# Performance work log

Hardware: AMD Instinct MI355X
Metric: run time of the kernel (lower is better)

The kernel has to match this reference:

```python
import jax, jax.numpy as jnp
import numpy as np

DIM = 768
N_HEADS = 12
HEAD_DIM = DIM // N_HEADS
B, T = 2, 2048


def setup_inputs() -> dict:
    key = jax.random.key(0)
    ks = jax.random.split(key, 11)
    s = 0.02
    return {
        "q_in": jax.random.normal(ks[0], (B, T, DIM), jnp.float32),
        "k_in": jax.random.normal(ks[1], (B, T, DIM), jnp.float32),
        "v_in": jax.random.normal(ks[2], (B, T, DIM), jnp.float32),
        "Wq": jax.random.normal(ks[3], (DIM, DIM), jnp.float32) * s,
        "bq": jnp.zeros((DIM,), jnp.float32),
        "Wk": jax.random.normal(ks[4], (DIM, DIM), jnp.float32) * s,
        "bk": jnp.zeros((DIM,), jnp.float32),
        "Wv": jax.random.normal(ks[5], (DIM, DIM), jnp.float32) * s,
        "bv": jnp.zeros((DIM,), jnp.float32),
        "Wo": jax.random.normal(ks[6], (DIM, DIM), jnp.float32) * s,
        "bo": jnp.zeros((DIM,), jnp.float32),
    }


def reference(q_in, k_in, v_in, Wq, bq, Wk, bk, Wv, bv, Wo, bo):
    b, t, c = q_in.shape
    scale = HEAD_DIM ** -0.5
    # linear projections (torch Linear: x @ W.T + b)
    q = q_in @ Wq.T + bq
    k = k_in @ Wk.T + bk
    v = v_in @ Wv.T + bv
    # [b, t, h, d] -> [b, h, t, d]
    q = q.reshape(b, t, N_HEADS, HEAD_DIM).transpose(0, 2, 1, 3)
    k = k.reshape(b, t, N_HEADS, HEAD_DIM).transpose(0, 2, 1, 3)
    v = v.reshape(b, t, N_HEADS, HEAD_DIM).transpose(0, 2, 1, 3)
    scores = jnp.einsum("bhqd,bhkd->bhqk", q, k) * scale  # full TxT scores
    probs = jax.nn.softmax(scores, axis=-1)
    attn = jnp.einsum("bhqk,bhkd->bhqd", probs, v)
    attn = attn.transpose(0, 2, 1, 3).reshape(b, t, c)
    return attn @ Wo.T + bo
```

## Files before the change

kernel.cpp:

```cpp
#include <hip/hip_runtime.h>


typedef unsigned short u16;
typedef __attribute__((ext_vector_type(8))) short short8;
typedef __attribute__((ext_vector_type(4))) short short4v;
typedef __attribute__((ext_vector_type(4))) float float4v;

#define DIMC 768
#define NTOK 4096
#define NHD  12
#define HDD  64
#define SEQT 2048

#if __has_builtin(__builtin_amdgcn_mfma_f32_16x16x16bf16_1k)
#define HAVE_MFMA16 1
#else
#define HAVE_MFMA16 0
#endif

__device__ __forceinline__ u16 f2bf(float f) {
  union { float f; unsigned u; } v; v.f = f;
  unsigned r = v.u + 0x7fffu + ((v.u >> 16) & 1u);
  return (u16)(r >> 16);
}
__device__ __forceinline__ float bf2f(u16 u) {
  union { unsigned u; float f; } v; v.u = ((unsigned)u) << 16;
  return v.f;
}
__device__ __forceinline__ short4v u2s4(uint2 u) {
  union { uint2 u; short4v s; } v; v.u = u; return v.s;
}

__global__ __launch_bounds__(256) void cvt_all(
    const float* __restrict__ a0, const float* __restrict__ a1, const float* __restrict__ a2,
    const float* __restrict__ a3, const float* __restrict__ a4, const float* __restrict__ a5,
    const float* __restrict__ a6,
    u16* __restrict__ o0, u16* __restrict__ o1, u16* __restrict__ o2,
    u16* __restrict__ o3, u16* __restrict__ o4, u16* __restrict__ o5,
    u16* __restrict__ o6) {
  int bid = blockIdx.x;
  const float* s; u16* d; int inner;
  if (bid < 9216) {
    int z = bid / 3072; inner = bid - z * 3072;
    s = (z == 0) ? a0 : (z == 1) ? a1 : a2;
    d = (z == 0) ? o0 : (z == 1) ? o1 : o2;
  } else {
    int r = bid - 9216; int z = r / 576; inner = r - z * 576;
    s = (z == 0) ? a3 : (z == 1) ? a4 : (z == 2) ? a5 : a6;
    d = (z == 0) ? o3 : (z == 1) ? o4 : (z == 2) ? o5 : o6;
  }
  size_t i = ((size_t)inner * 256 + threadIdx.x) * 4;
  float4 v = *(const float4*)(s + i);
  *(ushort4*)(d + i) = make_ushort4(f2bf(v.x), f2bf(v.y), f2bf(v.z), f2bf(v.w));
}

__device__ __forceinline__ void gemm_mainloop3(
    const u16* __restrict__ X, const u16* __restrict__ W,
    int m0, int n0, u16* Als, u16* Bls, float4v acc[4][4]) {
  int tid = threadIdx.x;
  int sr = tid >> 3, sc = (tid & 7) * 8;
  int w = tid >> 6, lane = tid & 63, quad = lane >> 4, r15 = lane & 15;
  int wm = (w >> 1) * 64, wn = (w & 1) * 64;
  const u16* xp0 = X + (size_t)(m0 + sr) * DIMC + sc;
  const u16* xp1 = xp0 + 32 * DIMC;
  const u16* xp2 = xp0 + 64 * DIMC;
  const u16* xp3 = xp0 + 96 * DIMC;
  const u16* wp0 = W + (size_t)(n0 + sr) * DIMC + sc;
  const u16* wp1 = wp0 + 32 * DIMC;
  const u16* wp2 = wp0 + 64 * DIMC;
  const u16* wp3 = wp0 + 96 * DIMC;
  uint4 pa0 = *(const uint4*)xp0, pa1 = *(const uint4*)xp1;
  uint4 pa2 = *(const uint4*)xp2, pa3 = *(const uint4*)xp3;
  uint4 pb0 = *(const uint4*)wp0, pb1 = *(const uint4*)wp1;
  uint4 pb2 = *(const uint4*)wp2, pb3 = *(const uint4*)wp3;
  for (int k0 = 0; k0 < DIMC; k0 += 64) {
    __syncthreads();
    *(uint4*)(Als + sr * 72 + sc) = pa0;
    *(uint4*)(Als + (sr + 32) * 72 + sc) = pa1;
    *(uint4*)(Als + (sr + 64) * 72 + sc) = pa2;
    *(uint4*)(Als + (sr + 96) * 72 + sc) = pa3;
    *(uint4*)(Bls + sr * 72 + sc) = pb0;
    *(uint4*)(Bls + (sr + 32) * 72 + sc) = pb1;
    *(uint4*)(Bls + (sr + 64) * 72 + sc) = pb2;
    *(uint4*)(Bls + (sr + 96) * 72 + sc) = pb3;
    __syncthreads();
    int kn = k0 + 64;
    if (kn < DIMC) {
      pa0 = *(const uint4*)(xp0 + kn); pa1 = *(const uint4*)(xp1 + kn);
      pa2 = *(const uint4*)(xp2 + kn); pa3 = *(const uint4*)(xp3 + kn);
      pb0 = *(const uint4*)(wp0 + kn); pb1 = *(const uint4*)(wp1 + kn);
      pb2 = *(const uint4*)(wp2 + kn); pb3 = *(const uint4*)(wp3 + kn);
    }
    #pragma unroll
    for (int sk = 0; sk < 2; sk++) {
      short8 af[4], bf[4];
      #pragma unroll
      for (int mf = 0; mf < 4; mf++)
        af[mf] = *(const short8*)(Als + (wm + mf * 16 + r15) * 72 + sk * 32 + quad * 8);
      #pragma unroll
      for (int nf = 0; nf < 4; nf++)
        bf[nf] = *(const short8*)(Bls + (wn + nf * 16 + r15) * 72 + sk * 32 + quad * 8);
      #pragma unroll
      for (int mf = 0; mf < 4; mf++)
        #pragma unroll
        for (int nf = 0; nf < 4; nf++)
          acc[mf][nf] = __builtin_amdgcn_mfma_f32_16x16x32_bf16(af[mf], bf[nf], acc[mf][nf], 0, 0, 0);
    }
  }
}

__global__ __launch_bounds__(256, 2) void gemm_qkv(
    const u16* __restrict__ xq, const u16* __restrict__ xk, const u16* __restrict__ xv,
    const u16* __restrict__ wq, const u16* __restrict__ wk, const u16* __restrict__ wv,
    const float* __restrict__ bq, const float* __restrict__ bk, const float* __restrict__ bv,
    u16* __restrict__ Qh, u16* __restrict__ Kh, u16* __restrict__ Vt) {
  __shared__ __align__(16) u16 LS[2 * 128 * 72];
  u16* Als = LS;
  u16* Bls = LS + 128 * 72;
  int z = blockIdx.z;
  const u16* X = (z == 0) ? xq : (z == 1) ? xk : xv;
  const u16* W = (z == 0) ? wq : (z == 1) ? wk : wv;
  const float* bias = (z == 0) ? bq : (z == 1) ? bk : bv;
  int m0 = blockIdx.x * 128, n0 = blockIdx.y * 128;
  float4v acc[4][4];
  #pragma unroll
  for (int i = 0; i < 4; i++)
    #pragma unroll
    for (int j = 0; j < 4; j++)
      #pragma unroll
      for (int r = 0; r < 4; r++) acc[i][j][r] = 0.f;
  gemm_mainloop3(X, W, m0, n0, Als, Bls, acc);
  int tid = threadIdx.x, w = tid >> 6, lane = tid & 63, quad = lane >> 4, r15 = lane & 15;
  int wm = (w >> 1) * 64, wn = (w & 1) * 64;
  if (z == 2) {
    __syncthreads();
    u16* T = LS;
    #pragma unroll
    for (int mf = 0; mf < 4; mf++)
      #pragma unroll
      for (int nf = 0; nf < 4; nf++)
        #pragma unroll
        for (int rg = 0; rg < 4; rg++) {
          int mloc = wm + mf * 16 + quad * 4 + rg;
          int nloc = wn + nf * 16 + r15;
          T[nloc * 136 + mloc] = f2bf(acc[mf][nf][rg] + bias[n0 + nloc]);
        }
    __syncthreads();
    int r = tid >> 1, seg = tid & 1;
    int b = m0 >> 11, t0 = m0 & 2047;
    int h = (n0 + r) >> 6, d = (n0 + r) & 63;
    size_t base = (((size_t)(b * NHD + h)) * HDD + d) * SEQT + t0 + seg * 64;
    const u16* src = T + r * 136 + seg * 64;
    #pragma unroll
    for (int j = 0; j < 8; j++)
      *(uint4*)(Vt + base + j * 8) = *(const uint4*)(src + j * 8);
  } else {
    #pragma unroll
    for (int mf = 0; mf < 4; mf++)
      #pragma unroll
      for (int nf = 0; nf < 4; nf++)
        #pragma unroll
        for (int rg = 0; rg < 4; rg++) {
          int m = m0 + wm + mf * 16 + quad * 4 + rg;
          int n = n0 + wn + nf * 16 + r15;
          float val = acc[mf][nf][rg] + bias[n];
          if (z == 0) val *= 0.180336880f;
          int b = m >> 11, t = m & 2047, h = n >> 6, d = n & 63;
          u16 o = f2bf(val);
          size_t bh = (size_t)(b * NHD + h);
          if (z == 0) Qh[(bh * SEQT + t) * HDD + d] = o;
          else Kh[(bh * SEQT + t) * HDD + d] = o;
        }
  }
}

__global__ __launch_bounds__(256, 4) void attn_kernel(
    const u16* __restrict__ Qh, const u16* __restrict__ Kh, const u16* __restrict__ Vt,
    u16* __restrict__ Opart, float* __restrict__ Lpart) {
  __shared__ __align__(16) u16 Kls[64 * 64];
  __shared__ __align__(16) u16 Vls[64 * 64];
#if !HAVE_MFMA16
  __shared__ __align__(16) u16 Pls[4 * 32 * 64];
#endif
  int bh = blockIdx.y, sp = blockIdx.z, qt0 = blockIdx.x * 128;
  int tid = threadIdx.x, w = tid >> 6, lane = tid & 63, quad = lane >> 4, r15 = lane & 15;
  int qw = qt0 + w * 32;
  const int nt = 8;
  int kt0 = sp * (nt * 64);

  int rr = r15 & 7;
  int sx0 = (quad ^ rr) * 8;
  int sx1 = ((4 + quad) ^ rr) * 8;
  int q1 = quad >> 1, q0 = quad & 1;

  short8 qa[2][2];
  #pragma unroll
  for (int qs = 0; qs < 2; qs++) {
    const u16* qp = Qh + ((size_t)bh * SEQT + qw + qs * 16 + r15) * HDD + quad * 8;
    qa[qs][0] = *(const short8*)qp;
    qa[qs][1] = *(const short8*)(qp + 32);
  }
  float4v fzero;
  #pragma unroll
  for (int r = 0; r < 4; r++) fzero[r] = 0.f;

  float4v oacc[2][4];
  float lsum[2];
  #pragma unroll
  for (int qs = 0; qs < 2; qs++) {
    lsum[qs] = 0.f;
    #pragma unroll
    for (int dt = 0; dt < 4; dt++)
      #pragma unroll
      for (int r = 0; r < 4; r++) oacc[qs][dt][r] = 0.f;
  }

  const u16* Kbase = Kh + (size_t)bh * SEQT * HDD;
  const u16* Vbase = Vt + (size_t)bh * HDD * SEQT;
  int sr = tid >> 3, sc = (tid & 7) * 8;
  int sg = (((tid & 7) ^ (sr & 7)) * 8);

  uint4 pk0 = *(const uint4*)(Kbase + (size_t)(kt0 + sr) * HDD + sc);
  uint4 pk1 = *(const uint4*)(Kbase + (size_t)(kt0 + sr + 32) * HDD + sc);
  uint4 pv0 = *(const uint4*)(Vbase + (size_t)sr * SEQT + kt0 + sc);
  uint4 pv1 = *(const uint4*)(Vbase + (size_t)(sr + 32) * SEQT + kt0 + sc);

  for (int it = 0; it < nt; it++) {
    __syncthreads();
    *(uint4*)(Kls + sr * 64 + sg) = pk0;
    *(uint4*)(Kls + (sr + 32) * 64 + sg) = pk1;
    *(uint4*)(Vls + sr * 64 + sg) = pv0;
    *(uint4*)(Vls + (sr + 32) * 64 + sg) = pv1;
    __syncthreads();
    int nit = it + 1; if (nit == nt) nit = 0;
    int ktn = kt0 + nit * 64;
    pk0 = *(const uint4*)(Kbase + (size_t)(ktn + sr) * HDD + sc);
    pk1 = *(const uint4*)(Kbase + (size_t)(ktn + sr + 32) * HDD + sc);
    pv0 = *(const uint4*)(Vbase + (size_t)sr * SEQT + ktn + sc);
    pv1 = *(const uint4*)(Vbase + (size_t)(sr + 32) * SEQT + ktn + sc);

    __builtin_amdgcn_s_setprio(1);
#if HAVE_MFMA16
    #pragma unroll
    for (int nk = 0; nk < 4; nk++) {
      short8 k0 = *(const short8*)(Kls + (nk * 16 + r15) * 64 + sx0);
      short8 k1 = *(const short8*)(Kls + (nk * 16 + r15) * 64 + sx1);
      #pragma unroll
      for (int qs = 0; qs < 2; qs++) {
        float4v zv = __builtin_amdgcn_mfma_f32_16x16x32_bf16(k0, qa[qs][0], fzero, 0, 0, 0);
        zv = __builtin_amdgcn_mfma_f32_16x16x32_bf16(k1, qa[qs][1], zv, 0, 0, 0);
        float p0 = __builtin_amdgcn_exp2f(zv[0]);
        float p1 = __builtin_amdgcn_exp2f(zv[1]);
        float p2 = __builtin_amdgcn_exp2f(zv[2]);
        float p3 = __builtin_amdgcn_exp2f(zv[3]);
        lsum[qs] += (p0 + p1) + (p2 + p3);
        uint2 pw = make_uint2(
            __builtin_amdgcn_perm(__float_as_uint(p1), __float_as_uint(p0), 0x07060302u),
            __builtin_amdgcn_perm(__float_as_uint(p3), __float_as_uint(p2), 0x07060302u));
        short4v pb = u2s4(pw);
        #pragma unroll
        for (int dt = 0; dt < 4; dt++) {
          uint2 vw = *(const uint2*)(Vls + (dt * 16 + r15) * 64 +
                                     (((nk * 2 + q1) ^ rr) * 8) + q0 * 4);
          oacc[qs][dt] = __builtin_amdgcn_mfma_f32_16x16x16bf16_1k(
              u2s4(vw), pb, oacc[qs][dt], 0, 0, 0);
        }
      }
    }
#else
    u16* Pw = Pls + w * (32 * 64);
    #pragma unroll
    for (int nk = 0; nk < 4; nk++) {
      short8 k0 = *(const short8*)(Kls + (nk * 16 + r15) * 64 + sx0);
      short8 k1 = *(const short8*)(Kls + (nk * 16 + r15) * 64 + sx1);
      #pragma unroll
      for (int qs = 0; qs < 2; qs++) {
        float4v zv = __builtin_amdgcn_mfma_f32_16x16x32_bf16(k0, qa[qs][0], fzero, 0, 0, 0);
        zv = __builtin_amdgcn_mfma_f32_16x16x32_bf16(k1, qa[qs][1], zv, 0, 0, 0);
        float p0 = __builtin_amdgcn_exp2f(zv[0]);
        float p1 = __builtin_amdgcn_exp2f(zv[1]);
        float p2 = __builtin_amdgcn_exp2f(zv[2]);
        float p3 = __builtin_amdgcn_exp2f(zv[3]);
        lsum[qs] += (p0 + p1) + (p2 + p3);
        unsigned lo = __builtin_amdgcn_perm(__float_as_uint(p1), __float_as_uint(p0), 0x07060302u);
        unsigned hi = __builtin_amdgcn_perm(__float_as_uint(p3), __float_as_uint(p2), 0x07060302u);
        *(uint2*)(Pw + (qs * 16 + r15) * 64 + (((nk * 4 + quad) ^ (rr << 1)) << 2)) =
            make_uint2(lo, hi);
      }
    }
    short8 pa[2][2];
    #pragma unroll
    for (int qs = 0; qs < 2; qs++) {
      pa[qs][0] = *(const short8*)(Pw + (qs * 16 + r15) * 64 + sx0);
      pa[qs][1] = *(const short8*)(Pw + (qs * 16 + r15) * 64 + sx1);
    }
    #pragma unroll
    for (int dt = 0; dt < 4; dt++) {
      short8 v0 = *(const short8*)(Vls + (dt * 16 + r15) * 64 + sx0);
      short8 v1 = *(const short8*)(Vls + (dt * 16 + r15) * 64 + sx1);
      #pragma unroll
      for (int qs = 0; qs < 2; qs++) {
        oacc[qs][dt] = __builtin_amdgcn_mfma_f32_16x16x32_bf16(pa[qs][0], v0, oacc[qs][dt], 0, 0, 0);
        oacc[qs][dt] = __builtin_amdgcn_mfma_f32_16x16x32_bf16(pa[qs][1], v1, oacc[qs][dt], 0, 0, 0);
      }
    }
#endif
    __builtin_amdgcn_s_setprio(0);
  }
  size_t obase = ((size_t)sp * 2 * NHD + bh) * SEQT + qw;
#if HAVE_MFMA16
  #pragma unroll
  for (int qs = 0; qs < 2; qs++) {
    u16* orow = Opart + (obase + qs * 16 + r15) * HDD + quad * 4;
    #pragma unroll
    for (int dt = 0; dt < 4; dt++) {
      u16 c0 = f2bf(oacc[qs][dt][0]);
      u16 c1 = f2bf(oacc[qs][dt][1]);
      u16 c2 = f2bf(oacc[qs][dt][2]);
      u16 c3 = f2bf(oacc[qs][dt][3]);
      *(uint2*)(orow + dt * 16) =
          make_uint2((unsigned)c0 | ((unsigned)c1 << 16),
                     (unsigned)c2 | ((unsigned)c3 << 16));
    }
  }
#else
  #pragma unroll
  for (int qs = 0; qs < 2; qs++)
    #pragma unroll
    for (int rg = 0; rg < 4; rg++) {
      u16* orow = Opart + (obase + qs * 16 + quad * 4 + rg) * HDD;
      #pragma unroll
      for (int dt = 0; dt < 4; dt++) orow[dt * 16 + r15] = f2bf(oacc[qs][dt][rg]);
    }
#endif
  #pragma unroll
  for (int qs = 0; qs < 2; qs++) {
    float s = lsum[qs];
    s += __shfl_xor(s, 16, 64);
    s += __shfl_xor(s, 32, 64);
    if (quad == 0) Lpart[obase + qs * 16 + r15] = s;
  }
}

__global__ __launch_bounds__(256) void merge_kernel(
    const u16* __restrict__ Opart, const float* __restrict__ Lpart, u16* __restrict__ X2) {
  const size_t NXe = (size_t)2 * NHD * SEQT * HDD;
  const size_t LS = (size_t)2 * NHD * SEQT;
  int tid = threadIdx.x;
  int row = blockIdx.x * 32 + (tid >> 3);
  int dcol = (tid & 7) * 8;
  int bh = row >> 11, t = row & 2047;
  size_t off = (size_t)row * HDD + dcol;
  float inv = 1.0f / (Lpart[row] + Lpart[row + LS] +
                      Lpart[row + 2 * LS] + Lpart[row + 3 * LS]);
  int b = bh / NHD, h = bh % NHD;
  u16 o[8];
  #pragma unroll
  for (int half = 0; half < 2; half++) {
    ushort4 a = *(const ushort4*)(Opart + off + half * 4);
    ushort4 c = *(const ushort4*)(Opart + off + NXe + half * 4);
    ushort4 e = *(const ushort4*)(Opart + off + 2 * NXe + half * 4);
    ushort4 g = *(const ushort4*)(Opart + off + 3 * NXe + half * 4);
    o[half * 4 + 0] = f2bf((bf2f(a.x) + bf2f(c.x) + bf2f(e.x) + bf2f(g.x)) * inv);
    o[half * 4 + 1] = f2bf((bf2f(a.y) + bf2f(c.y) + bf2f(e.y) + bf2f(g.y)) * inv);
    o[half * 4 + 2] = f2bf((bf2f(a.z) + bf2f(c.z) + bf2f(e.z) + bf2f(g.z)) * inv);
    o[half * 4 + 3] = f2bf((bf2f(a.w) + bf2f(c.w) + bf2f(e.w) + bf2f(g.w)) * inv);
  }
  *(uint4*)(X2 + ((size_t)b * SEQT + t) * DIMC + h * HDD + dcol) = *(uint4*)o;
}

__global__ __launch_bounds__(256, 2) void gemm_out(
    const u16* __restrict__ X2, const u16* __restrict__ wo,
    const float* __restrict__ bo, float* __restrict__ out) {
  __shared__ __align__(16) u16 LS[2 * 128 * 72];
  u16* Als = LS;
  u16* Bls = LS + 128 * 72;
  int m0 = blockIdx.x * 128, n0 = blockIdx.y * 128;
  float4v acc[4][4];
  #pragma unroll
  for (int i = 0; i < 4; i++)
    #pragma unroll
    for (int j = 0; j < 4; j++)
      #pragma unroll
      for (int r = 0; r < 4; r++) acc[i][j][r] = 0.f;
  gemm_mainloop3(X2, wo, m0, n0, Als, Bls, acc);
  int tid = threadIdx.x, w = tid >> 6, lane = tid & 63, quad = lane >> 4, r15 = lane & 15;
  int wm = (w >> 1) * 64, wn = (w & 1) * 64;
  #pragma unroll
  for (int mf = 0; mf < 4; mf++)
    #pragma unroll
    for (int nf = 0; nf < 4; nf++)
      #pragma unroll
      for (int rg = 0; rg < 4; rg++) {
        int m = m0 + wm + mf * 16 + quad * 4 + rg;
        int n = n0 + wn + nf * 16 + r15;
        out[(size_t)m * DIMC + n] = acc[mf][nf][rg] + bo[n];
      }
}

extern "C" void kernel_launch(void* const* d_in, const int* in_sizes, int n_in,
                              void* d_out, int out_size, void* d_ws, size_t ws_size,
                              hipStream_t stream) {
  const float* q_in = (const float*)d_in[0];
  const float* k_in = (const float*)d_in[1];
  const float* v_in = (const float*)d_in[2];
  const float* Wq = (const float*)d_in[3];
  const float* bq = (const float*)d_in[4];
  const float* Wk = (const float*)d_in[5];
  const float* bk = (const float*)d_in[6];
  const float* Wv = (const float*)d_in[7];
  const float* bv = (const float*)d_in[8];
  const float* Wo = (const float*)d_in[9];
  const float* bo = (const float*)d_in[10];

  const size_t NX = (size_t)NTOK * DIMC;
  const size_t NW = (size_t)DIMC * DIMC;
  u16* ws = (u16*)d_ws;
  u16* qb = ws;
  u16* kb = qb + NX;
  u16* vb = kb + NX;
  u16* wqb = vb + NX;
  u16* wkb = wqb + NW;
  u16* wvb = wkb + NW;
  u16* wob = wvb + NW;
  u16* Qh = wob + NW;
  u16* Kh = Qh + NX;
  u16* Vt = Kh + NX;
  u16* X2 = Vt + NX;
  u16* Opart = X2 + NX;
  float* Lpart = (float*)(Opart + 4 * NX);

  cvt_all<<<dim3(11520), 256, 0, stream>>>(
      q_in, k_in, v_in, Wq, Wk, Wv, Wo, qb, kb, vb, wqb, wkb, wvb, wob);
  gemm_qkv<<<dim3(NTOK / 128, DIMC / 128, 3), 256, 0, stream>>>(
      qb, kb, vb, wqb, wkb, wvb, bq, bk, bv, Qh, Kh, Vt);
  attn_kernel<<<dim3(SEQT / 128, 2 * NHD, 4), 256, 0, stream>>>(Qh, Kh, Vt, Opart, Lpart);
  merge_kernel<<<dim3(2 * NHD * SEQT / 32), 256, 0, stream>>>(Opart, Lpart, X2);
  gemm_out<<<dim3(NTOK / 128, DIMC / 128), 256, 0, stream>>>(X2, wob, bo, (float*)d_out);
}
```

Baseline: 189.8 us.

## Fuse split-K attention merge into output projection GEMM and interleave PV MFMAs

After: 239.9 us. 1.26x slower.

```diff
diff --git a/kernel.cpp b/kernel.cpp
--- a/kernel.cpp
+++ b/kernel.cpp
@@ -245,26 +245,33 @@
     for (int nk = 0; nk < 4; nk++) {
       short8 k0 = *(const short8*)(Kls + (nk * 16 + r15) * 64 + sx0);
       short8 k1 = *(const short8*)(Kls + (nk * 16 + r15) * 64 + sx1);
-      #pragma unroll
-      for (int qs = 0; qs < 2; qs++) {
-        float4v zv = __builtin_amdgcn_mfma_f32_16x16x32_bf16(k0, qa[qs][0], fzero, 0, 0, 0);
-        zv = __builtin_amdgcn_mfma_f32_16x16x32_bf16(k1, qa[qs][1], zv, 0, 0, 0);
-        float p0 = __builtin_amdgcn_exp2f(zv[0]);
-        float p1 = __builtin_amdgcn_exp2f(zv[1]);
-        float p2 = __builtin_amdgcn_exp2f(zv[2]);
-        float p3 = __builtin_amdgcn_exp2f(zv[3]);
-        lsum[qs] += (p0 + p1) + (p2 + p3);
-        uint2 pw = make_uint2(
-            __builtin_amdgcn_perm(__float_as_uint(p1), __float_as_uint(p0), 0x07060302u),
-            __builtin_amdgcn_perm(__float_as_uint(p3), __float_as_uint(p2), 0x07060302u));
-        short4v pb = u2s4(pw);
-        #pragma unroll
-        for (int dt = 0; dt < 4; dt++) {
-          uint2 vw = *(const uint2*)(Vls + (dt * 16 + r15) * 64 +
-                                     (((nk * 2 + q1) ^ rr) * 8) + q0 * 4);
-          oacc[qs][dt] = __builtin_amdgcn_mfma_f32_16x16x16bf16_1k(
-              u2s4(vw), pb, oacc[qs][dt], 0, 0, 0);
-        }
+      float4v z0 = __builtin_amdgcn_mfma_f32_16x16x32_bf16(k0, qa[0][0], fzero, 0, 0, 0);
+      z0 = __builtin_amdgcn_mfma_f32_16x16x32_bf16(k1, qa[0][1], z0, 0, 0, 0);
+      float4v z1 = __builtin_amdgcn_mfma_f32_16x16x32_bf16(k0, qa[1][0], fzero, 0, 0, 0);
+      z1 = __builtin_amdgcn_mfma_f32_16x16x32_bf16(k1, qa[1][1], z1, 0, 0, 0);
+      float a0 = __builtin_amdgcn_exp2f(z0[0]);
+      float a1 = __builtin_amdgcn_exp2f(z0[1]);
+      float a2 = __builtin_amdgcn_exp2f(z0[2]);
+      float a3 = __builtin_amdgcn_exp2f(z0[3]);
+      float b0 = __builtin_amdgcn_exp2f(z1[0]);
+      float b1 = __builtin_amdgcn_exp2f(z1[1]);
+      float b2 = __builtin_amdgcn_exp2f(z1[2]);
+      float b3 = __builtin_amdgcn_exp2f(z1[3]);
+      lsum[0] += (a0 + a1) + (a2 + a3);
+      lsum[1] += (b0 + b1) + (b2 + b3);
+      short4v pb0 = u2s4(make_uint2(
+          __builtin_amdgcn_perm(__float_as_uint(a1), __float_as_uint(a0), 0x07060302u),
+          __builtin_amdgcn_perm(__float_as_uint(a3), __float_as_uint(a2), 0x07060302u)));
+      short4v pb1 = u2s4(make_uint2(
+          __builtin_amdgcn_perm(__float_as_uint(b1), __float_as_uint(b0), 0x07060302u),
+          __builtin_amdgcn_perm(__float_as_uint(b3), __float_as_uint(b2), 0x07060302u)));
+      #pragma unroll
+      for (int dt = 0; dt < 4; dt++) {
+        uint2 vw = *(const uint2*)(Vls + (dt * 16 + r15) * 64 +
+                                   (((nk * 2 + q1) ^ rr) * 8) + q0 * 4);
+        short4v va = u2s4(vw);
+        oacc[0][dt] = __builtin_amdgcn_mfma_f32_16x16x16bf16_1k(va, pb0, oacc[0][dt], 0, 0, 0);
+        oacc[1][dt] = __builtin_amdgcn_mfma_f32_16x16x16bf16_1k(va, pb1, oacc[1][dt], 0, 0, 0);
       }
     }
 #else
@@ -342,40 +349,51 @@
   }
 }
 
-__global__ __launch_bounds__(256) void merge_kernel(
-    const u16* __restrict__ Opart, const float* __restrict__ Lpart, u16* __restrict__ X2) {
-  const size_t NXe = (size_t)2 * NHD * SEQT * HDD;
-  const size_t LS = (size_t)2 * NHD * SEQT;
-  int tid = threadIdx.x;
-  int row = blockIdx.x * 32 + (tid >> 3);
-  int dcol = (tid & 7) * 8;
-  int bh = row >> 11, t = row & 2047;
-  size_t off = (size_t)row * HDD + dcol;
-  float inv = 1.0f / (Lpart[row] + Lpart[row + LS] +
-                      Lpart[row + 2 * LS] + Lpart[row + 3 * LS]);
-  int b = bh / NHD, h = bh % NHD;
-  u16 o[8];
-  #pragma unroll
-  for (int half = 0; half < 2; half++) {
-    ushort4 a = *(const ushort4*)(Opart + off + half * 4);
-    ushort4 c = *(const ushort4*)(Opart + off + NXe + half * 4);
-    ushort4 e = *(const ushort4*)(Opart + off + 2 * NXe + half * 4);
-    ushort4 g = *(const ushort4*)(Opart + off + 3 * NXe + half * 4);
-    o[half * 4 + 0] = f2bf((bf2f(a.x) + bf2f(c.x) + bf2f(e.x) + bf2f(g.x)) * inv);
-    o[half * 4 + 1] = f2bf((bf2f(a.y) + bf2f(c.y) + bf2f(e.y) + bf2f(g.y)) * inv);
-    o[half * 4 + 2] = f2bf((bf2f(a.z) + bf2f(c.z) + bf2f(e.z) + bf2f(g.z)) * inv);
-    o[half * 4 + 3] = f2bf((bf2f(a.w) + bf2f(c.w) + bf2f(e.w) + bf2f(g.w)) * inv);
-  }
-  *(uint4*)(X2 + ((size_t)b * SEQT + t) * DIMC + h * HDD + dcol) = *(uint4*)o;
-}
-
-__global__ __launch_bounds__(256, 2) void gemm_out(
-    const u16* __restrict__ X2, const u16* __restrict__ wo,
-    const float* __restrict__ bo, float* __restrict__ out) {
+__device__ __forceinline__ unsigned mergew(unsigned a, unsigned c, unsigned e,
+                                           unsigned g, float inv) {
+  float lo = (bf2f((u16)a) + bf2f((u16)c) + bf2f((u16)e) + bf2f((u16)g)) * inv;
+  float hi = (bf2f((u16)(a >> 16)) + bf2f((u16)(c >> 16)) +
+              bf2f((u16)(e >> 16)) + bf2f((u16)(g >> 16))) * inv;
+  return (unsigned)f2bf(lo) | ((unsigned)f2bf(hi) << 16);
+}
+
+__device__ __forceinline__ uint4 mergeA(const u16* __restrict__ Opart,
+                                        const float* __restrict__ Lpart,
+                                        int bh, int t, int sc) {
+  const size_t NXs = (size_t)2 * NHD * SEQT * HDD;
+  const size_t LSz = (size_t)2 * NHD * SEQT;
+  size_t lrow = (size_t)bh * SEQT + t;
+  float inv = 1.0f / (Lpart[lrow] + Lpart[lrow + LSz] +
+                      Lpart[lrow + 2 * LSz] + Lpart[lrow + 3 * LSz]);
+  size_t off = lrow * HDD + sc;
+  uint4 a = *(const uint4*)(Opart + off);
+  uint4 c = *(const uint4*)(Opart + off + NXs);
+  uint4 e = *(const uint4*)(Opart + off + 2 * NXs);
+  uint4 g = *(const uint4*)(Opart + off + 3 * NXs);
+  uint4 o;
+  o.x = mergew(a.x, c.x, e.x, g.x, inv);
+  o.y = mergew(a.y, c.y, e.y, g.y, inv);
+  o.z = mergew(a.z, c.z, e.z, g.z, inv);
+  o.w = mergew(a.w, c.w, e.w, g.w, inv);
+  return o;
+}
+
+__global__ __launch_bounds__(256, 2) void gemm_out_fused(
+    const u16* __restrict__ Opart, const float* __restrict__ Lpart,
+    const u16* __restrict__ wo, const float* __restrict__ bo, float* __restrict__ out) {
   __shared__ __align__(16) u16 LS[2 * 128 * 72];
   u16* Als = LS;
   u16* Bls = LS + 128 * 72;
+  int tid = threadIdx.x;
+  int sr = tid >> 3, sc = (tid & 7) * 8;
+  int w = tid >> 6, lane = tid & 63, quad = lane >> 4, r15 = lane & 15;
+  int wm = (w >> 1) * 64, wn = (w & 1) * 64;
   int m0 = blockIdx.x * 128, n0 = blockIdx.y * 128;
+  int b = m0 >> 11, t0 = m0 & 2047;
+  const u16* wp0 = wo + (size_t)(n0 + sr) * DIMC + sc;
+  const u16* wp1 = wp0 + 32 * DIMC;
+  const u16* wp2 = wp0 + 64 * DIMC;
+  const u16* wp3 = wp0 + 96 * DIMC;
   float4v acc[4][4];
   #pragma unroll
   for (int i = 0; i < 4; i++)
@@ -383,9 +401,49 @@
     for (int j = 0; j < 4; j++)
       #pragma unroll
       for (int r = 0; r < 4; r++) acc[i][j][r] = 0.f;
-  gemm_mainloop3(X2, wo, m0, n0, Als, Bls, acc);
-  int tid = threadIdx.x, w = tid >> 6, lane = tid & 63, quad = lane >> 4, r15 = lane & 15;
-  int wm = (w >> 1) * 64, wn = (w & 1) * 64;
+  uint4 pa0 = mergeA(Opart, Lpart, b * NHD, t0 + sr, sc);
+  uint4 pa1 = mergeA(Opart, Lpart, b * NHD, t0 + sr + 32, sc);
+  uint4 pa2 = mergeA(Opart, Lpart, b * NHD, t0 + sr + 64, sc);
+  uint4 pa3 = mergeA(Opart, Lpart, b * NHD, t0 + sr + 96, sc);
+  uint4 pb0 = *(const uint4*)wp0, pb1 = *(const uint4*)wp1;
+  uint4 pb2 = *(const uint4*)wp2, pb3 = *(const uint4*)wp3;
+  for (int k0 = 0; k0 < DIMC; k0 += 64) {
+    __syncthreads();
+    *(uint4*)(Als + sr * 72 + sc) = pa0;
+    *(uint4*)(Als + (sr + 32) * 72 + sc) = pa1;
+    *(uint4*)(Als + (sr + 64) * 72 + sc) = pa2;
+    *(uint4*)(Als + (sr + 96) * 72 + sc) = pa3;
+    *(uint4*)(Bls + sr * 72 + sc) = pb0;
+    *(uint4*)(Bls + (sr + 32) * 72 + sc) = pb1;
+    *(uint4*)(Bls + (sr + 64) * 72 + sc) = pb2;
+    *(uint4*)(Bls + (sr + 96) * 72 + sc) = pb3;
+    __syncthreads();
+    int kn = k0 + 64;
+    if (kn < DIMC) {
+      int hn = kn >> 6;
+      pa0 = mergeA(Opart, Lpart, b * NHD + hn, t0 + sr, sc);
+      pa1 = mergeA(Opart, Lpart, b * NHD + hn, t0 + sr + 32, sc);
+      pa2 = mergeA(Opart, Lpart, b * NHD + hn, t0 + sr + 64, sc);
+      pa3 = mergeA(Opart, Lpart, b * NHD + hn, t0 + sr + 96, sc);
+      pb0 = *(const uint4*)(wp0 + kn); pb1 = *(const uint4*)(wp1 + kn);
+      pb2 = *(const uint4*)(wp2 + kn); pb3 = *(const uint4*)(wp3 + kn);
+    }
+    #pragma unroll
+    for (int sk = 0; sk < 2; sk++) {
+      short8 af[4], bf[4];
+      #pragma unroll
+      for (int mf = 0; mf < 4; mf++)
+        af[mf] = *(const short8*)(Als + (wm + mf * 16 + r15) * 72 + sk * 32 + quad * 8);
+      #pragma unroll
+      for (int nf = 0; nf < 4; nf++)
+        bf[nf] = *(const short8*)(Bls + (wn + nf * 16 + r15) * 72 + sk * 32 + quad * 8);
+      #pragma unroll
+      for (int mf = 0; mf < 4; mf++)
+        #pragma unroll
+        for (int nf = 0; nf < 4; nf++)
+          acc[mf][nf] = __builtin_amdgcn_mfma_f32_16x16x32_bf16(af[mf], bf[nf], acc[mf][nf], 0, 0, 0);
+    }
+  }
   #pragma unroll
   for (int mf = 0; mf < 4; mf++)
     #pragma unroll
@@ -435,6 +493,6 @@
   gemm_qkv<<<dim3(NTOK / 128, DIMC / 128, 3), 256, 0, stream>>>(
       qb, kb, vb, wqb, wkb, wvb, bq, bk, bv, Qh, Kh, Vt);
   attn_kernel<<<dim3(SEQT / 128, 2 * NHD, 4), 256, 0, stream>>>(Qh, Kh, Vt, Opart, Lpart);
-  merge_kernel<<<dim3(2 * NHD * SEQT / 32), 256, 0, stream>>>(Opart, Lpart, X2);
-  gemm_out<<<dim3(NTOK / 128, DIMC / 128), 256, 0, stream>>>(X2, wob, bo, (float*)d_out);
-}
+  gemm_out_fused<<<dim3(NTOK / 128, DIMC / 128), 256, 0, stream>>>(
+      Opart, Lpart, wob, bo, (float*)d_out);
+}
```
